# Kernel optimization log

Measured on AMD Instinct MI355X. Metric: run time of the kernel, lower is better.

Reference implementation:

```python
import jax, jax.numpy as jnp
import numpy as np
from jax import lax

ALPHA = 2.0
T_TAGS = 8  # number of distinct connects tags
ANCHOR_POS_FACTOR = jnp.array([1.0, 1.0], dtype=jnp.float32)
POS_FACTOR = [2.0, 1.0]  # [4,4,4,2,1][-2:]
NEG_FACTOR = [2.0, 1.0]


def setup_inputs() -> dict:
    key = jax.random.key(0)
    ks = jax.random.split(key, 10)
    B, A, M = 2, 2, 64
    Da, Db = 128, 64
    logits_a = jax.random.normal(ks[0], (B, A, Da, Da, Da), dtype=jnp.float32)
    logits_b = jax.random.normal(ks[1], (B, A, Db, Db, Db), dtype=jnp.float32)
    # GT prob maps: background labeled -1 (negmask), sparse positives labeled 1
    prob_a = jnp.where(jax.random.uniform(ks[2], (B, A, Da, Da, Da)) < 0.995, -1.0, 1.0).astype(jnp.float32)
    prob_b = jnp.where(jax.random.uniform(ks[3], (B, A, Db, Db, Db)) < 0.995, -1.0, 1.0).astype(jnp.float32)
    connects_a = jax.random.randint(ks[4], (B, A, Da, Da, Da), 0, T_TAGS, dtype=jnp.int32)
    connects_b = jax.random.randint(ks[5], (B, A, Db, Db, Db), 0, T_TAGS, dtype=jnp.int32)
    def make_coord(k, D):
        ka, kz = jax.random.split(k)
        anc = jax.random.randint(ka, (B, M, 1), 0, A, dtype=jnp.int32)
        sp = jax.random.randint(kz, (B, M, 3), 0, D, dtype=jnp.int32)
        c = jnp.concatenate([anc, sp], axis=-1)
        # pad last quarter of rows with -1 (invalid), as in the original padded coord lists
        c = c.at[:, 3 * M // 4:, :].set(-1)
        return c
    coord_a = make_coord(ks[6], Da)
    coord_b = make_coord(ks[7], Db)
    fnames = jnp.arange(B, dtype=jnp.float32)
    return {"logits_a": logits_a, "logits_b": logits_b, "prob_a": prob_a, "prob_b": prob_b,
            "connects_a": connects_a, "connects_b": connects_b,
            "coord_a": coord_a, "coord_b": coord_b, "fnames": fnames}


def _level_loss(logits, prob_gt, connects, coord, pos_f, neg_f):
    # ---- negative branch: sigmoid/logsigmoid elementwise + NMS maxpool mask ----
    prob = jax.nn.sigmoid(logits)
    nll = -jax.nn.log_sigmoid(-logits)  # -log(1 - sigmoid(logit))
    negmask = (prob_gt == -1.0).astype(logits.dtype)
    # max_pool3d kernel 3, stride 1, pad 1 over (D,H,W); anchors are channels
    pooled = lax.reduce_window(prob, -jnp.inf, lax.max,
                               (1, 1, 3, 3, 3), (1, 1, 1, 1, 1), 'SAME')
    max_filter = lax.stop_gradient((pooled == prob).astype(logits.dtype))
    negmask = negmask * max_filter
    w_neg = lax.stop_gradient(prob) ** ALPHA * negmask
    loss_neg = jnp.sum(nll * w_neg) * neg_f
    count_neg = jnp.sum(w_neg)
    wsum_neg = jnp.sum(w_neg) * neg_f

    # ---- positive branch: batched gather at coords (pad rows = -1) ----
    B, M, _ = coord.shape
    valid = coord[:, :, 0] > -1                       # [B, M]
    c = jnp.where(valid[..., None], coord, 0)         # safe indices
    b_idx = jnp.arange(B)[:, None]
    lp = logits[b_idx, c[..., 0], c[..., 1], c[..., 2], c[..., 3]]  # [B, M]
    pp = jax.nn.sigmoid(lp)
    w1 = (1.0 - lax.stop_gradient(pp)) ** ALPHA
    w2 = ANCHOR_POS_FACTOR[c[..., 0]]
    vf = valid.astype(logits.dtype)
    loss_pos = -jnp.sum(jax.nn.log_sigmoid(lp) * w1 * w2 * vf) * pos_f
    count_pos = jnp.sum(w1 * vf)
    wsum_pos = jnp.sum(w1 * w2 * vf) * pos_f

    # ---- connects-tag segment-min grouping (torch.unique + per-tag min) ----
    tags = connects[b_idx, c[..., 0], c[..., 1], c[..., 2], c[..., 3]]  # [B, M]
    seg = (jnp.arange(B, dtype=jnp.int32)[:, None] * T_TAGS + tags).reshape(-1)
    data = jnp.where(valid, w1, jnp.inf).reshape(-1)
    seg_min = jax.ops.segment_min(data, seg, num_segments=B * T_TAGS).reshape(B, T_TAGS)
    seg_min = jnp.where(jnp.isfinite(seg_min), seg_min, -1.0)  # absent tags -> -1 sentinel
    return loss_pos, loss_neg, count_pos, count_neg, wsum_pos, wsum_neg, seg_min


def reference(logits_a, logits_b, prob_a, prob_b, connects_a, connects_b, coord_a, coord_b, fnames):
    ra = _level_loss(logits_a, prob_a, connects_a, coord_a, POS_FACTOR[0], NEG_FACTOR[0])
    rb = _level_loss(logits_b, prob_b, connects_b, coord_b, POS_FACTOR[1], NEG_FACTOR[1])
    cls_loss_pos = ra[0] + rb[0]
    cls_loss_neg = ra[1] + rb[1]
    count_pos = ra[2] + rb[2]
    count_neg = ra[3] + rb[3]
    wsum_pos = ra[4] + rb[4]
    wsum_neg = ra[5] + rb[5]
    # pred_prob summary: per (level, sample, tag) min positive weight; fnames broadcast alongside
    pred_prob_min = jnp.stack([ra[6], rb[6]], axis=0)  # [2, B, T_TAGS]
    return (cls_loss_pos, cls_loss_neg, count_pos, count_neg, wsum_pos, wsum_neg, pred_prob_min)
```

## Files before the change

### kernel.cpp

```cpp
#include <hip/hip_runtime.h>
#include <math.h>


#define NBLK_A 1024
#define NBLK_B 128
#define NBLK_TOTAL (NBLK_A + NBLK_B + 1)

__device__ __forceinline__ float fmax3(float a, float b, float c) {
    return fmaxf(a, fmaxf(b, c));
}

template <int D, int LOG2D, int XQ>
__device__ __forceinline__ void neg_march(
    const float* __restrict__ logits, const float* __restrict__ gt,
    int vol, int z, int y0, int xq, float& loss, float& wsum)
{
    const int x0 = xq << 2;
    const float* vb = logits + (vol << (3 * LOG2D));
    const int zm = z > 0 ? z - 1 : 0;
    const int zp = z < D - 1 ? z + 1 : z;
    const float* pzm = vb + (zm << (2 * LOG2D));
    const float* pz0 = vb + (z << (2 * LOG2D));
    const float* pzp = vb + (zp << (2 * LOG2D));
    const float* pg = gt + (vol << (3 * LOG2D)) + (z << (2 * LOG2D));

    float zw[3][4];
    float cc[2][4];
    float4 gg[2];

#pragma unroll
    for (int s = 0; s < 10; ++s) {
        int yy = y0 - 1 + s;
        yy = yy < 0 ? 0 : (yy > D - 1 ? D - 1 : yy);
        const int ro = (yy << LOG2D) + x0;
        float4 r0 = *(const float4*)(pzm + ro);
        float4 r1 = *(const float4*)(pz0 + ro);
        float4 r2 = *(const float4*)(pzp + ro);
        if (s >= 1 && s <= 8) gg[s & 1] = *(const float4*)(pg + ro);
        zw[s % 3][0] = fmax3(r0.x, r1.x, r2.x);
        zw[s % 3][1] = fmax3(r0.y, r1.y, r2.y);
        zw[s % 3][2] = fmax3(r0.z, r1.z, r2.z);
        zw[s % 3][3] = fmax3(r0.w, r1.w, r2.w);
        cc[s & 1][0] = r1.x; cc[s & 1][1] = r1.y;
        cc[s & 1][2] = r1.z; cc[s & 1][3] = r1.w;
        if (s >= 2) {
            float cz0 = fmax3(zw[0][0], zw[1][0], zw[2][0]);
            float cz1 = fmax3(zw[0][1], zw[1][1], zw[2][1]);
            float cz2 = fmax3(zw[0][2], zw[1][2], zw[2][2]);
            float cz3 = fmax3(zw[0][3], zw[1][3], zw[2][3]);
            float lco = __shfl_up(cz3, 1);   if (xq == 0)      lco = cz0;
            float rco = __shfl_down(cz0, 1); if (xq == XQ - 1) rco = cz3;
            float m0 = fmax3(lco, cz0, cz1);
            float m1 = fmax3(cz0, cz1, cz2);
            float m2 = fmax3(cz1, cz2, cz3);
            float m3 = fmax3(cz2, cz3, rco);
            const float* c = cc[(s - 1) & 1];
            float4 gq = gg[(s - 1) & 1];
            float ms[4] = {m0, m1, m2, m3};
            float gs[4] = {gq.x, gq.y, gq.z, gq.w};
#pragma unroll
            for (int k = 0; k < 4; ++k) {
                if (gs[k] == -1.0f && ms[k] == c[k]) {
                    float e = __expf(c[k]);
                    float u = __builtin_amdgcn_rcpf(1.0f + e);
                    float sc = e * u;
                    float wv = sc * sc;
                    wsum += wv;
                    loss += (-__logf(u)) * wv;
                }
            }
        }
    }
}

__global__ __launch_bounds__(256, 4) void fused_kernel(
    const float* __restrict__ la, const float* __restrict__ lb,
    const float* __restrict__ ga, const float* __restrict__ gb,
    const int* __restrict__ conn_a, const int* __restrict__ conn_b,
    const int* __restrict__ coord_a, const int* __restrict__ coord_b,
    float* __restrict__ ws, float* __restrict__ out)
{
    __shared__ float sred[8];
    __shared__ float w1s[128];
    __shared__ float tgf[128];
    const int bid = blockIdx.x;
    const int t = threadIdx.x;
    float loss = 0.0f, wsum = 0.0f;
    int accIdx = -1;

    if (bid < NBLK_A) {
        accIdx = 0;
        const int c = bid & 7;
        const int g = bid >> 3;
        const int yc = g & 15;
        const int j = g >> 4;
        const int vol = j >> 1;
        const int zb = ((j & 1) << 3) | c;
        neg_march<128, 7, 32>(la, ga, vol, zb * 8 + (t >> 5), yc * 8, t & 31,
                              loss, wsum);
    } else if (bid < NBLK_A + NBLK_B) {
        accIdx = 2;
        const int b2 = bid - NBLK_A;
        const int vol = b2 >> 5;
        const int rem = b2 & 31;
        const int zb = rem >> 3, yc = rem & 7;
        neg_march<64, 6, 16>(lb, gb, vol, zb * 16 + (t >> 4), yc * 8, t & 15,
                             loss, wsum);
    } else {
        for (int level = 0; level < 2; ++level) {
            const float* logits = level ? lb : la;
            const int* conn = level ? conn_b : conn_a;
            const int* coord = level ? coord_b : coord_a;
            const int D = level ? 64 : 128;
            float li = 0.0f, ci = 0.0f;
            if (t < 128) {
                const int* c4 = coord + t * 4;
                int a = c4[0], zz = c4[1], yy = c4[2], xx = c4[3];
                bool valid = a > -1;
                int aa = valid ? a : 0, z2 = valid ? zz : 0,
                    y2 = valid ? yy : 0, x2 = valid ? xx : 0;
                int b = t >> 6;
                int off = (((b * 2 + aa) * D + z2) * D + y2) * D + x2;
                float lp = logits[off];
                int tag = conn[off];
                float s = 1.0f / (1.0f + expf(lp));
                float w1 = s * s;
                float vf = valid ? 1.0f : 0.0f;
                float sp = fmaxf(-lp, 0.0f) + log1pf(expf(-fabsf(lp)));
                li = sp * w1 * vf;
                ci = w1 * vf;
                w1s[t] = w1;
                tgf[t] = (float)(valid ? tag : -1);
            }
            for (int o = 32; o; o >>= 1) {
                li += __shfl_down(li, o);
                ci += __shfl_down(ci, o);
            }
            if ((t & 63) == 0) { sred[t >> 6] = li; sred[4 + (t >> 6)] = ci; }
            __syncthreads();
            if (t == 0) {
                atomicAdd(ws + 4 + 2 * level, sred[0] + sred[1] + sred[2] + sred[3]);
                atomicAdd(ws + 5 + 2 * level, sred[4] + sred[5] + sred[6] + sred[7]);
            }
            if (t < 16) {
                int bb = t >> 3, tg = t & 7;
                float mn = INFINITY;
                for (int i = 0; i < 64; ++i) {
                    int j = bb * 64 + i;
                    if (tgf[j] == (float)tg) mn = fminf(mn, w1s[j]);
                }
                out[6 + level * 16 + bb * 8 + tg] = isinf(mn) ? -1.0f : mn;
            }
            __syncthreads();
        }
    }

    if (accIdx >= 0) {
        for (int o = 32; o; o >>= 1) {
            loss += __shfl_down(loss, o);
            wsum += __shfl_down(wsum, o);
        }
        if ((t & 63) == 0) { sred[t >> 6] = loss; sred[4 + (t >> 6)] = wsum; }
        __syncthreads();
        if (t == 0) {
            float L = sred[0] + sred[1] + sred[2] + sred[3];
            float W = sred[4] + sred[5] + sred[6] + sred[7];
            if (L != 0.0f || W != 0.0f) {
                atomicAdd(ws + accIdx, L);
                atomicAdd(ws + accIdx + 1, W);
            }
        }
    }

    if (t == 0) {
        __threadfence();
        unsigned int old = atomicAdd((unsigned int*)(ws + 8), 1u);
        if (old == NBLK_TOTAL - 1) {
            float s0 = atomicAdd(ws + 0, 0.0f);
            float s1 = atomicAdd(ws + 1, 0.0f);
            float s2 = atomicAdd(ws + 2, 0.0f);
            float s3 = atomicAdd(ws + 3, 0.0f);
            float s4 = atomicAdd(ws + 4, 0.0f);
            float s5 = atomicAdd(ws + 5, 0.0f);
            float s6 = atomicAdd(ws + 6, 0.0f);
            float s7 = atomicAdd(ws + 7, 0.0f);
            out[0] = s4 * 2.0f + s6;
            out[1] = s0 * 2.0f + s2;
            out[2] = s5 + s7;
            out[3] = s1 + s3;
            out[4] = s5 * 2.0f + s7;
            out[5] = s1 * 2.0f + s3;
        }
    }
}

extern "C" void kernel_launch(void* const* d_in, const int* in_sizes, int n_in,
                              void* d_out, int out_size, void* d_ws, size_t ws_size,
                              hipStream_t stream) {
    const float* logits_a = (const float*)d_in[0];
    const float* logits_b = (const float*)d_in[1];
    const float* prob_a   = (const float*)d_in[2];
    const float* prob_b   = (const float*)d_in[3];
    const int*   conn_a   = (const int*)d_in[4];
    const int*   conn_b   = (const int*)d_in[5];
    const int*   coord_a  = (const int*)d_in[6];
    const int*   coord_b  = (const int*)d_in[7];
    float* out = (float*)d_out;
    float* ws  = (float*)d_ws;

    hipMemsetAsync(ws, 0, 12 * sizeof(float), stream);
    fused_kernel<<<NBLK_TOTAL, 256, 0, stream>>>(
        logits_a, logits_b, prob_a, prob_b,
        conn_a, conn_b, coord_a, coord_b, ws, out);
}
```

Before: 182.3 us.

## Stage 3D max-pool halo tiles in LDS via global_load_lds

```diff
diff --git a/kernel.cpp b/kernel.cpp
--- a/kernel.cpp
+++ b/kernel.cpp
@@ -2,47 +2,76 @@
 #include <math.h>
 
 
-#define NBLK_A 1024
-#define NBLK_B 128
+#define NBLK_A 2048
+#define NBLK_B 256
 #define NBLK_TOTAL (NBLK_A + NBLK_B + 1)
 
 __device__ __forceinline__ float fmax3(float a, float b, float c) {
     return fmaxf(a, fmaxf(b, c));
 }
 
-template <int D, int LOG2D, int XQ>
-__device__ __forceinline__ void neg_march(
+__device__ __forceinline__ void load_lds_16(const float* g, float* l) {
+    __builtin_amdgcn_global_load_lds(
+        (const __attribute__((address_space(1))) void*)g,
+        (__attribute__((address_space(3))) void*)l,
+        16, 0, 0);
+}
+
+template <int D, int LOG2D, int XQ, int RZ, int ZI>
+__device__ __forceinline__ void neg_tile(
     const float* __restrict__ logits, const float* __restrict__ gt,
-    int vol, int z, int y0, int xq, float& loss, float& wsum)
+    float* __restrict__ tile, int vol, int z0, int y0, int t,
+    float& loss, float& wsum)
 {
+    constexpr int QPR = D >> 2;
+    constexpr int QPR_SH = LOG2D - 2;
+    constexpr int NROWS = RZ * 6;
+    constexpr int NQ = NROWS * QPR;
+    constexpr int ITERS = (NQ + 255) / 256;
+    const float* vb = logits + (vol << (3 * LOG2D));
+
+#pragma unroll
+    for (int i = 0; i < ITERS; ++i) {
+        int u = i * 256 + t;
+        if (u < NQ) {
+            int r = u >> QPR_SH;
+            int q = u & (QPR - 1);
+            int rz = r / 6;
+            int ry = r - rz * 6;
+            int gz = z0 - 1 + rz; gz = gz < 0 ? 0 : (gz > D - 1 ? D - 1 : gz);
+            int gy = y0 - 1 + ry; gy = gy < 0 ? 0 : (gy > D - 1 ? D - 1 : gy);
+            load_lds_16(vb + (gz << (2 * LOG2D)) + (gy << LOG2D) + (q << 2),
+                        tile + u * 4);
+        }
+    }
+
+    const int xq = t & (XQ - 1);
+    const int zi = t / XQ;
     const int x0 = xq << 2;
-    const float* vb = logits + (vol << (3 * LOG2D));
-    const int zm = z > 0 ? z - 1 : 0;
-    const int zp = z < D - 1 ? z + 1 : z;
-    const float* pzm = vb + (zm << (2 * LOG2D));
-    const float* pz0 = vb + (z << (2 * LOG2D));
-    const float* pzp = vb + (zp << (2 * LOG2D));
-    const float* pg = gt + (vol << (3 * LOG2D)) + (z << (2 * LOG2D));
-
+    const float* pg = gt + (vol << (3 * LOG2D)) + ((z0 + zi) << (2 * LOG2D)) + x0;
+    float4 gq[4];
+#pragma unroll
+    for (int j = 0; j < 4; ++j)
+        gq[j] = *(const float4*)(pg + ((y0 + j) << LOG2D));
+
+    __syncthreads();
+
+    const float* tz0 = tile + ((zi + 0) * 6) * D + x0;
+    const float* tz1 = tile + ((zi + 1) * 6) * D + x0;
+    const float* tz2 = tile + ((zi + 2) * 6) * D + x0;
     float zw[3][4];
     float cc[2][4];
-    float4 gg[2];
-
-#pragma unroll
-    for (int s = 0; s < 10; ++s) {
-        int yy = y0 - 1 + s;
-        yy = yy < 0 ? 0 : (yy > D - 1 ? D - 1 : yy);
-        const int ro = (yy << LOG2D) + x0;
-        float4 r0 = *(const float4*)(pzm + ro);
-        float4 r1 = *(const float4*)(pz0 + ro);
-        float4 r2 = *(const float4*)(pzp + ro);
-        if (s >= 1 && s <= 8) gg[s & 1] = *(const float4*)(pg + ro);
-        zw[s % 3][0] = fmax3(r0.x, r1.x, r2.x);
-        zw[s % 3][1] = fmax3(r0.y, r1.y, r2.y);
-        zw[s % 3][2] = fmax3(r0.z, r1.z, r2.z);
-        zw[s % 3][3] = fmax3(r0.w, r1.w, r2.w);
-        cc[s & 1][0] = r1.x; cc[s & 1][1] = r1.y;
-        cc[s & 1][2] = r1.z; cc[s & 1][3] = r1.w;
+#pragma unroll
+    for (int s = 0; s < 6; ++s) {
+        float4 a0 = *(const float4*)(tz0 + s * D);
+        float4 a1 = *(const float4*)(tz1 + s * D);
+        float4 a2 = *(const float4*)(tz2 + s * D);
+        zw[s % 3][0] = fmax3(a0.x, a1.x, a2.x);
+        zw[s % 3][1] = fmax3(a0.y, a1.y, a2.y);
+        zw[s % 3][2] = fmax3(a0.z, a1.z, a2.z);
+        zw[s % 3][3] = fmax3(a0.w, a1.w, a2.w);
+        cc[s & 1][0] = a1.x; cc[s & 1][1] = a1.y;
+        cc[s & 1][2] = a1.z; cc[s & 1][3] = a1.w;
         if (s >= 2) {
             float cz0 = fmax3(zw[0][0], zw[1][0], zw[2][0]);
             float cz1 = fmax3(zw[0][1], zw[1][1], zw[2][1]);
@@ -55,9 +84,9 @@
             float m2 = fmax3(cz1, cz2, cz3);
             float m3 = fmax3(cz2, cz3, rco);
             const float* c = cc[(s - 1) & 1];
-            float4 gq = gg[(s - 1) & 1];
+            float4 gv = gq[s - 2];
             float ms[4] = {m0, m1, m2, m3};
-            float gs[4] = {gq.x, gq.y, gq.z, gq.w};
+            float gs[4] = {gv.x, gv.y, gv.z, gv.w};
 #pragma unroll
             for (int k = 0; k < 4; ++k) {
                 if (gs[k] == -1.0f && ms[k] == c[k]) {
@@ -80,9 +109,8 @@
     const int* __restrict__ coord_a, const int* __restrict__ coord_b,
     float* __restrict__ ws, float* __restrict__ out)
 {
+    __shared__ float tile[7680];
     __shared__ float sred[8];
-    __shared__ float w1s[128];
-    __shared__ float tgf[128];
     const int bid = blockIdx.x;
     const int t = threadIdx.x;
     float loss = 0.0f, wsum = 0.0f;
@@ -92,21 +120,27 @@
         accIdx = 0;
         const int c = bid & 7;
         const int g = bid >> 3;
-        const int yc = g & 15;
-        const int j = g >> 4;
+        const int yc = g & 31;
+        const int j = g >> 5;
         const int vol = j >> 1;
         const int zb = ((j & 1) << 3) | c;
-        neg_march<128, 7, 32>(la, ga, vol, zb * 8 + (t >> 5), yc * 8, t & 31,
-                              loss, wsum);
+        neg_tile<128, 7, 32, 10, 8>(la, ga, tile, vol, zb * 8, yc * 4, t,
+                                    loss, wsum);
     } else if (bid < NBLK_A + NBLK_B) {
         accIdx = 2;
         const int b2 = bid - NBLK_A;
-        const int vol = b2 >> 5;
-        const int rem = b2 & 31;
-        const int zb = rem >> 3, yc = rem & 7;
-        neg_march<64, 6, 16>(lb, gb, vol, zb * 16 + (t >> 4), yc * 8, t & 15,
-                             loss, wsum);
+        const int c = b2 & 7;
+        const int g = b2 >> 3;
+        const int yc = g & 15;
+        const int j = g >> 4;
+        const int unit = c * 2 + j;
+        const int vol = unit >> 2;
+        const int zb = unit & 3;
+        neg_tile<64, 6, 16, 18, 16>(lb, gb, tile, vol, zb * 16, yc * 4, t,
+                                    loss, wsum);
     } else {
+        float* w1s = tile;
+        float* tgf = tile + 128;
         for (int level = 0; level < 2; ++level) {
             const float* logits = level ? lb : la;
             const int* conn = level ? conn_b : conn_a;
@@ -146,8 +180,8 @@
                 int bb = t >> 3, tg = t & 7;
                 float mn = INFINITY;
                 for (int i = 0; i < 64; ++i) {
-                    int j = bb * 64 + i;
-                    if (tgf[j] == (float)tg) mn = fminf(mn, w1s[j]);
+                    int j2 = bb * 64 + i;
+                    if (tgf[j2] == (float)tg) mn = fminf(mn, w1s[j2]);
                 }
                 out[6 + level * 16 + bb * 8 + tg] = isinf(mn) ? -1.0f : mn;
             }
```

Result: slower. 229.4 us (+25.8%).
